# Optimization experiments

Hardware: AMD Instinct MI355X
Metric: run time of the kernel (lower is better)

## Reference

```python
import jax, jax.numpy as jnp
import numpy as np

N, K, E = 262144, 8, 16
DT = 0.02  # config.delta_time


def _mono(x, w1, b1, w2, b2):
    # monotonic_fun with increasing=False: out_linear(exp(-in_linear(x)))
    return jnp.exp(-(x @ w1.T + b1)) @ w2.T + b2


def _isin(a, b):
    # rowwise torch.isin: a [N,P], b [N,Q] -> [N,P] bool
    return (a[:, :, None] == b[:, None, :]).any(-1)


def _angle_clamp(vec, v, ang):
    # torch.cosine_similarity(v, vec, dim=-1).abs() > ang gate (eps=1e-8)
    num = jnp.einsum('nd,nrd->nr', v, vec)
    den = jnp.maximum(jnp.linalg.norm(v, axis=-1)[:, None] * jnp.linalg.norm(vec, axis=-1), 1e-8)
    keep = jnp.abs(num / den) > ang
    return jnp.where(keep[..., None], vec, 0.0)


def _linear_params(key, fan_in, fan_out):
    a = 1.0 / np.sqrt(fan_in)
    k1, k2 = jax.random.split(key)
    # weightConstraint(min_b=0) clamps weights to >= 0 at init
    w = jnp.maximum(jax.random.uniform(k1, (fan_out, fan_in), minval=-a, maxval=a), 0.0)
    b = jax.random.uniform(k2, (fan_out,), minval=-a, maxval=a)
    return w, b


def _mono_params(key):
    k1, k2 = jax.random.split(key)
    w1, b1 = _linear_params(k1, 1, E)
    w2, b2 = _linear_params(k2, E, 1)
    return w1, b1, w2, b2


def setup_inputs() -> dict:
    key = jax.random.key(0)
    ks = jax.random.split(key, 12)
    ego = jax.random.normal(ks[0], (N, 16), dtype=jnp.float32)
    ego = ego.at[:, 0].set(jnp.arange(N, dtype=jnp.float32))
    # surrounding-vehicle id columns 7..14 as small integer ids (floats)
    ego = ego.at[:, 7:15].set(jax.random.randint(ks[1], (N, 8), 0, 21).astype(jnp.float32))
    nei = jax.random.normal(ks[2], (N, K, 16), dtype=jnp.float32)
    nei = nei.at[:, :, 0].set(jax.random.randint(ks[3], (N, K), 1, 21).astype(jnp.float32))
    border = jax.random.uniform(ks[4], (4,), dtype=jnp.float32) * 10.0 + 1.0
    recording_time = jnp.zeros((N, K, 2), dtype=jnp.float32)
    p_dest = jax.random.uniform(ks[5], (2,), dtype=jnp.float32)  # relu(rand(2))
    angle = jax.nn.sigmoid(jax.random.uniform(ks[6], (1,), dtype=jnp.float32))
    d = {'ego': ego, 'nei': nei, 'border': border, 'recording_time': recording_time,
         'p_dest': p_dest, 'angle': angle}
    for name, kk in (('rep', ks[7]), ('att', ks[8]), ('bor', ks[9]), ('del', ks[10])):
        w1, b1, w2, b2 = _mono_params(kk)
        d[name + '_w1'], d[name + '_b1'], d[name + '_w2'], d[name + '_b2'] = w1, b1, w2, b2
    return d


def reference(ego, nei, border, recording_time, p_dest, angle,
              rep_w1, rep_b1, rep_w2, rep_b2,
              att_w1, att_b1, att_w2, att_b2,
              bor_w1, bor_b1, bor_w2, bor_b2,
              del_w1, del_b1, del_w2, del_b2):
    ang = angle[0]
    v = ego[:, 3:5]                                        # ego velocity [N,2]
    speed = jnp.linalg.norm(v, axis=-1)
    desired = jnp.stack([speed, jnp.zeros_like(speed)], axis=1)
    f_dest = ((p_dest[1] * desired - v) / p_dest[0])[:, None, :]   # [N,1,2]

    nei_id = nei[:, :, 0]                                  # [N,K]
    idx = _isin(nei_id, ego[:, 7:15]) & (nei_id != 0)

    # --- recording_time buffer update (vectorized remain/new/pad concat) ---
    buf_id, buf_ct = recording_time[:, :, 0], recording_time[:, :, 1]
    ifin = _isin(buf_id, nei_id)                           # buffer slots still present
    ct2 = buf_ct + ifin.astype(buf_ct.dtype)               # increment their counts
    ifnew = (~_isin(nei_id, buf_id)) & (nei_id != 0)       # brand-new neighbor ids
    cand = jnp.concatenate([jnp.stack([buf_id, ct2], -1),
                            jnp.stack([nei_id, jnp.ones_like(nei_id)], -1)], axis=1)  # [N,2K,2]
    ar = jnp.arange(K)
    BIG = 1 << 20
    keyord = jnp.concatenate([jnp.where(ifin, ar, BIG), jnp.where(ifnew, ar + K, BIG)], axis=1)
    order = jnp.argsort(keyord, axis=1)[:, :K]             # stable: remain order, then new, then pad
    skey = jnp.take_along_axis(keyord, order, axis=1)
    new_buf = jnp.where((skey < BIG)[..., None],
                        jnp.take_along_axis(cand, order[..., None], axis=1), 1.0)  # pad with ones
    count = new_buf[:, :, 1]                               # [N,K]

    # --- neighbor attraction / repulsion ---
    r = jnp.where(idx[..., None], nei[:, :, 1:3] - ego[:, None, 1:3], 0.0)
    rn = jnp.linalg.norm(r, axis=-1)
    rns = jnp.where(idx, rn, 1.0)                          # safe divisor (masked slots zeroed below)
    dirn = r / rns[..., None]
    f_attr = (_mono(count[..., None], del_w1, del_b1, del_w2, del_b2)
              * _mono(rn[..., None], att_w1, att_b1, att_w2, att_b2) * dirn)
    v_nei = nei[:, :, 3:5]
    b = rn + jnp.sum((r + v_nei * DT) ** 2, -1) - jnp.sum((v_nei * DT) ** 2, -1)
    b = jnp.sqrt(jnp.maximum(jnp.where(idx, b, 1.0), 1e-12)) / 2.0
    f_repu = _mono(b[..., None], rep_w1, rep_b1, rep_w2, rep_b2) * dirn
    f_attr = jnp.where(idx[..., None], f_attr, 0.0)
    f_repu = jnp.where(idx[..., None], f_repu, 0.0)

    # --- border repulsion (y-axis only), select_lane = [0, -1] ---
    rb_all = ego[:, 2:3] - border                          # [N,4]
    rb = jnp.stack([rb_all[:, 0], rb_all[:, -1]], axis=1)  # [N,2]
    rbn = jnp.abs(rb)
    f_by = _mono(rbn[..., None], bor_w1, bor_b1, bor_w2, bor_b2) * (rb / rbn)[..., None]
    f_bor = jnp.concatenate([jnp.zeros_like(f_by), f_by], axis=-1)  # [N,2,2]

    f_destination = _angle_clamp(f_dest, v, ang).sum(1)
    f_neighbors = _angle_clamp(f_attr, v, ang).sum(1) + _angle_clamp(f_repu, v, ang).sum(1)
    f_border = _angle_clamp(f_bor, v, ang).sum(1)
    return jnp.stack([f_destination, f_neighbors, f_border], axis=1)  # [N,3,2]
```

## Files before the change

### kernel.cpp

```cpp
#include <hip/hip_runtime.h>
#include <math.h>

#define KN 8
#define EN 16

__device__ __forceinline__ float mono_eval(float x,
    const float* __restrict__ w1, const float* __restrict__ b1,
    const float* __restrict__ w2, float b2) {
    float acc = 0.0f;
#pragma unroll
    for (int e = 0; e < EN; ++e) {
        float pre = x * w1[e] + b1[e];
        acc += expf(-pre) * w2[e];
    }
    return acc + b2;
}

__device__ __forceinline__ void clamp_add(float vx, float vy, float vnorm, float ang,
                                          float fx, float fy, float& ax, float& ay) {
    float num = vx * fx + vy * fy;
    float fn  = sqrtf(fx * fx + fy * fy);
    float den = fmaxf(vnorm * fn, 1e-8f);
    float c   = num / den;
    if (fabsf(c) > ang) { ax += fx; ay += fy; }
}

extern "C" __global__ void __launch_bounds__(256)
sfm_kernel(const float* __restrict__ ego, const float* __restrict__ nei,
           const float* __restrict__ border, const float* __restrict__ rec,
           const float* __restrict__ p_dest, const float* __restrict__ angle,
           const float* __restrict__ rep_w1, const float* __restrict__ rep_b1,
           const float* __restrict__ rep_w2, const float* __restrict__ rep_b2,
           const float* __restrict__ att_w1, const float* __restrict__ att_b1,
           const float* __restrict__ att_w2, const float* __restrict__ att_b2,
           const float* __restrict__ bor_w1, const float* __restrict__ bor_b1,
           const float* __restrict__ bor_w2, const float* __restrict__ bor_b2,
           const float* __restrict__ del_w1, const float* __restrict__ del_b1,
           const float* __restrict__ del_w2, const float* __restrict__ del_b2,
           float* __restrict__ out, int N)
{
    int n = blockIdx.x * blockDim.x + threadIdx.x;
    if (n >= N) return;

    const float ang = angle[0];
    const float p0 = p_dest[0], p1 = p_dest[1];
    const float b0 = border[0], b3 = border[3];

    const float4* e4 = (const float4*)(ego + (size_t)n * 16);
    float4 ea = e4[0], eb = e4[1], ec = e4[2], ed = e4[3];
    const float px_e = ea.y, py_e = ea.z;
    const float vx = ea.w, vy = eb.x;
    float egid[8] = {eb.w, ec.x, ec.y, ec.z, ec.w, ed.x, ed.y, ed.z};

    const float speed = sqrtf(vx * vx + vy * vy);

    float fdx = (p1 * speed - vx) / p0;
    float fdy = (0.0f - vy) / p0;
    float fdestx = 0.0f, fdesty = 0.0f;
    clamp_add(vx, vy, speed, ang, fdx, fdy, fdestx, fdesty);

    const float* nb = nei + (size_t)n * (KN * 16);
    float nid[KN], nx_[KN], ny_[KN], nvx[KN], nvy[KN];
#pragma unroll
    for (int k = 0; k < KN; ++k) {
        float4 a = *(const float4*)(nb + k * 16);
        nid[k] = a.x; nx_[k] = a.y; ny_[k] = a.z; nvx[k] = a.w;
        nvy[k] = nb[k * 16 + 4];
    }

    const float* rbuf = rec + (size_t)n * (KN * 2);
    float bid[KN], bct[KN];
#pragma unroll
    for (int k = 0; k < KN; k += 2) {
        float4 t = *(const float4*)(rbuf + k * 2);
        bid[k] = t.x; bct[k] = t.y; bid[k + 1] = t.z; bct[k + 1] = t.w;
    }

    float cnt[KN];
#pragma unroll
    for (int k = 0; k < KN; ++k) cnt[k] = 1.0f;
    int slot = 0;
#pragma unroll
    for (int k = 0; k < KN; ++k) {
        bool fin = false;
#pragma unroll
        for (int j = 0; j < KN; ++j) fin |= (bid[k] == nid[j]);
        if (fin) {
            float v2 = bct[k] + 1.0f;
#pragma unroll
            for (int s = 0; s < KN; ++s) if (slot == s) cnt[s] = v2;
            slot++;
        }
    }
#pragma unroll
    for (int k = 0; k < KN; ++k) {
        bool inbuf = false;
#pragma unroll
        for (int j = 0; j < KN; ++j) inbuf |= (nid[k] == bid[j]);
        bool isnew = (!inbuf) && (nid[k] != 0.0f);
        if (isnew) {
#pragma unroll
            for (int s = 0; s < KN; ++s) if (slot == s) cnt[s] = 1.0f;
            slot++;
        }
    }

    const float del_one = mono_eval(1.0f, del_w1, del_b1, del_w2, del_b2[0]);

    float fax_acc = 0.0f, fay_acc = 0.0f;
    float frx_acc = 0.0f, fry_acc = 0.0f;
#pragma unroll
    for (int k = 0; k < KN; ++k) {
        bool match = false;
#pragma unroll
        for (int j = 0; j < 8; ++j) match |= (nid[k] == egid[j]);
        const bool idxk = match && (nid[k] != 0.0f);

        float rx = idxk ? (nx_[k] - px_e) : 0.0f;
        float ry = idxk ? (ny_[k] - py_e) : 0.0f;
        float rn = sqrtf(rx * rx + ry * ry);
        float rns = idxk ? rn : 1.0f;
        float dx = rx / rns, dy = ry / rns;

        float att = mono_eval(rn, att_w1, att_b1, att_w2, att_b2[0]);
        float del = (cnt[k] == 1.0f) ? del_one
                  : mono_eval(cnt[k], del_w1, del_b1, del_w2, del_b2[0]);
        float fax = del * att * dx;
        float fay = del * att * dy;
        if (!idxk) { fax = 0.0f; fay = 0.0f; }
        clamp_add(vx, vy, speed, ang, fax, fay, fax_acc, fay_acc);

        float sx = nvx[k] * 0.02f, sy = nvy[k] * 0.02f;
        float ox = rx + sx, oy = ry + sy;
        float bsum = rn + (ox * ox + oy * oy) - (sx * sx + sy * sy);
        float bgate = idxk ? bsum : 1.0f;
        float bb = sqrtf(fmaxf(bgate, 1e-12f)) / 2.0f;

        float rep = mono_eval(bb, rep_w1, rep_b1, rep_w2, rep_b2[0]);
        float frx = rep * dx, fry = rep * dy;
        if (!idxk) { frx = 0.0f; fry = 0.0f; }
        clamp_add(vx, vy, speed, ang, frx, fry, frx_acc, fry_acc);
    }

    float fbx_acc = 0.0f, fby_acc = 0.0f;
    float rbv0 = py_e - b0, rbv1 = py_e - b3;
#pragma unroll
    for (int r = 0; r < 2; ++r) {
        float rb = (r == 0) ? rbv0 : rbv1;
        float rbn = fabsf(rb);
        float m = mono_eval(rbn, bor_w1, bor_b1, bor_w2, bor_b2[0]);
        float fby = m * (rb / rbn);
        clamp_add(vx, vy, speed, ang, 0.0f, fby, fbx_acc, fby_acc);
    }

    float2* o = (float2*)(out + (size_t)n * 6);
    o[0] = make_float2(fdestx, fdesty);
    o[1] = make_float2(fax_acc + frx_acc, fay_acc + fry_acc);
    o[2] = make_float2(fbx_acc, fby_acc);
}

extern "C" void kernel_launch(void* const* d_in, const int* in_sizes, int n_in,
                              void* d_out, int out_size, void* d_ws, size_t ws_size,
                              hipStream_t stream) {
    const float* ego    = (const float*)d_in[0];
    const float* nei    = (const float*)d_in[1];
    const float* border = (const float*)d_in[2];
    const float* rec    = (const float*)d_in[3];
    const float* p_dest = (const float*)d_in[4];
    const float* angle  = (const float*)d_in[5];
    const float* rep_w1 = (const float*)d_in[6];
    const float* rep_b1 = (const float*)d_in[7];
    const float* rep_w2 = (const float*)d_in[8];
    const float* rep_b2 = (const float*)d_in[9];
    const float* att_w1 = (const float*)d_in[10];
    const float* att_b1 = (const float*)d_in[11];
    const float* att_w2 = (const float*)d_in[12];
    const float* att_b2 = (const float*)d_in[13];
    const float* bor_w1 = (const float*)d_in[14];
    const float* bor_b1 = (const float*)d_in[15];
    const float* bor_w2 = (const float*)d_in[16];
    const float* bor_b2 = (const float*)d_in[17];
    const float* del_w1 = (const float*)d_in[18];
    const float* del_b1 = (const float*)d_in[19];
    const float* del_w2 = (const float*)d_in[20];
    const float* del_b2 = (const float*)d_in[21];
    float* out = (float*)d_out;

    int N = in_sizes[0] / 16;
    dim3 grid((N + 255) / 256);
    sfm_kernel<<<grid, 256, 0, stream>>>(
        ego, nei, border, rec, p_dest, angle,
        rep_w1, rep_b1, rep_w2, rep_b2,
        att_w1, att_b1, att_w2, att_b2,
        bor_w1, bor_b1, bor_w2, bor_b2,
        del_w1, del_b1, del_w2, del_b2,
        out, N);
}
```

Baseline: 268.0 us.

## Split each agent across 8 lanes, one neighbor per lane, with wave shuffles

Maps one thread per (agent, neighbor) pair instead of one thread per agent. The recording-buffer count compaction now uses ballot/popc/shuffle, and the per-agent sums are reduced with xor shuffles. The goal is 8x more parallelism and coalesced neighbor loads for a kernel bound by transcendentals and latency. The exp calls also switch to fast __expf with fma, which trades some accuracy. Each lane redundantly reloads the ego row, and the count-1 shortcut for the del network is dropped, so every lane evaluates it.

```diff
diff --git a/kernel.cpp b/kernel.cpp
--- a/kernel.cpp
+++ b/kernel.cpp
@@ -1,28 +1,18 @@
 #include <hip/hip_runtime.h>
 #include <math.h>
 
-#define KN 8
 #define EN 16
 
-__device__ __forceinline__ float mono_eval(float x,
+__device__ __forceinline__ float mono_fast(float x,
     const float* __restrict__ w1, const float* __restrict__ b1,
-    const float* __restrict__ w2, float b2) {
+    const float* __restrict__ w2, const float* __restrict__ b2) {
     float acc = 0.0f;
 #pragma unroll
     for (int e = 0; e < EN; ++e) {
-        float pre = x * w1[e] + b1[e];
-        acc += expf(-pre) * w2[e];
+        float pre = fmaf(x, w1[e], b1[e]);
+        acc = fmaf(__expf(-pre), w2[e], acc);
     }
-    return acc + b2;
-}
-
-__device__ __forceinline__ void clamp_add(float vx, float vy, float vnorm, float ang,
-                                          float fx, float fy, float& ax, float& ay) {
-    float num = vx * fx + vy * fy;
-    float fn  = sqrtf(fx * fx + fy * fy);
-    float den = fmaxf(vnorm * fn, 1e-8f);
-    float c   = num / den;
-    if (fabsf(c) > ang) { ax += fx; ay += fy; }
+    return acc + b2[0];
 }
 
 extern "C" __global__ void __launch_bounds__(256)
@@ -39,124 +29,125 @@
            const float* __restrict__ del_w2, const float* __restrict__ del_b2,
            float* __restrict__ out, int N)
 {
-    int n = blockIdx.x * blockDim.x + threadIdx.x;
+    const int gid = blockIdx.x * blockDim.x + threadIdx.x;
+    const int n = gid >> 3;
+    const int k = gid & 7;
     if (n >= N) return;
+    const int lane = threadIdx.x & 63;
+    const int gbase = lane & ~7;
 
     const float ang = angle[0];
     const float p0 = p_dest[0], p1 = p_dest[1];
-    const float b0 = border[0], b3 = border[3];
 
-    const float4* e4 = (const float4*)(ego + (size_t)n * 16);
-    float4 ea = e4[0], eb = e4[1], ec = e4[2], ed = e4[3];
-    const float px_e = ea.y, py_e = ea.z;
-    const float vx = ea.w, vy = eb.x;
-    float egid[8] = {eb.w, ec.x, ec.y, ec.z, ec.w, ed.x, ed.y, ed.z};
+    const float* er = ego + (size_t)n * 16;
+    float4 ea = *(const float4*)(er);
+    float4 eb = *(const float4*)(er + 4);
+    float4 ec = *(const float4*)(er + 8);
+    float4 ed = *(const float4*)(er + 12);
+    const float px = ea.y, py = ea.z, vx = ea.w, vy = eb.x;
+    const float speed = sqrtf(vx * vx + vy * vy);
 
-    const float speed = sqrtf(vx * vx + vy * vy);
+    const float* nb = nei + (size_t)n * 128 + (size_t)k * 16;
+    float4 na = *(const float4*)nb;
+    const float nvyv = nb[4];
+    const float nid = na.x;
+
+    float2 rc = *(const float2*)(rec + (size_t)n * 16 + (size_t)k * 2);
+    const float bid = rc.x, bct = rc.y;
+
+    bool fin = (bid == nid);
+#pragma unroll
+    for (int t = 1; t < 8; ++t)
+        fin = fin || (bid == __shfl_xor(nid, t));
+
+    unsigned long long bal = __ballot(fin);
+    unsigned finM = (unsigned)((bal >> gbase) & 0xFFull);
+    int popcFin = __popc(finM);
+    int jsel = 0, cbits = 0;
+#pragma unroll
+    for (int j = 0; j < 8; ++j) {
+        int bit = (finM >> j) & 1;
+        if (bit && cbits == k) jsel = j;
+        cbits += bit;
+    }
+    float bctj = __shfl(bct, gbase + jsel);
+    float cntk = (k < popcFin) ? (bctj + 1.0f) : 1.0f;
+
+    bool match = (nid == eb.w) || (nid == ec.x) || (nid == ec.y) || (nid == ec.z)
+              || (nid == ec.w) || (nid == ed.x) || (nid == ed.y) || (nid == ed.z);
+    const bool idxk = match && (nid != 0.0f);
+
+    float rx = idxk ? (na.y - px) : 0.0f;
+    float ry = idxk ? (na.z - py) : 0.0f;
+    float rn = sqrtf(rx * rx + ry * ry);
+    float rns = idxk ? rn : 1.0f;
+    float dx = rx / rns, dy = ry / rns;
+
+    float att = mono_fast(rn,   att_w1, att_b1, att_w2, att_b2);
+    float del = mono_fast(cntk, del_w1, del_b1, del_w2, del_b2);
+    float sa = del * att;
+    float fax = idxk ? sa * dx : 0.0f;
+    float fay = idxk ? sa * dy : 0.0f;
+
+    float nbx = 0.0f, nby = 0.0f;
+    {
+        float num = vx * fax + vy * fay;
+        float fn = sqrtf(fax * fax + fay * fay);
+        float den = fmaxf(speed * fn, 1e-8f);
+        if (fabsf(num / den) > ang) { nbx += fax; nby += fay; }
+    }
+
+    float sxv = na.w * 0.02f, syv = nvyv * 0.02f;
+    float ox = rx + sxv, oy = ry + syv;
+    float bsum = rn + (ox * ox + oy * oy) - (sxv * sxv + syv * syv);
+    float bgate = idxk ? bsum : 1.0f;
+    float bb = sqrtf(fmaxf(bgate, 1e-12f)) * 0.5f;
+    float rep = mono_fast(bb, rep_w1, rep_b1, rep_w2, rep_b2);
+    float frx = idxk ? rep * dx : 0.0f;
+    float fry = idxk ? rep * dy : 0.0f;
+    {
+        float num = vx * frx + vy * fry;
+        float fn = sqrtf(frx * frx + fry * fry);
+        float den = fmaxf(speed * fn, 1e-8f);
+        if (fabsf(num / den) > ang) { nbx += frx; nby += fry; }
+    }
+
+    float bsel = (k == 0) ? border[0] : border[3];
+    float rb = py - bsel;
+    float rbn = fabsf(rb);
+    float mb = mono_fast(rbn, bor_w1, bor_b1, bor_w2, bor_b2);
+    float fby = mb * (rb / rbn);
+    float bory = 0.0f;
+    {
+        float num = vy * fby;
+        float den = fmaxf(speed * fabsf(fby), 1e-8f);
+        if ((fabsf(num / den) > ang) && (k < 2)) bory = fby;
+    }
+
+#pragma unroll
+    for (int m = 1; m < 8; m <<= 1) {
+        nbx  += __shfl_xor(nbx,  m);
+        nby  += __shfl_xor(nby,  m);
+        bory += __shfl_xor(bory, m);
+    }
 
     float fdx = (p1 * speed - vx) / p0;
     float fdy = (0.0f - vy) / p0;
-    float fdestx = 0.0f, fdesty = 0.0f;
-    clamp_add(vx, vy, speed, ang, fdx, fdy, fdestx, fdesty);
-
-    const float* nb = nei + (size_t)n * (KN * 16);
-    float nid[KN], nx_[KN], ny_[KN], nvx[KN], nvy[KN];
-#pragma unroll
-    for (int k = 0; k < KN; ++k) {
-        float4 a = *(const float4*)(nb + k * 16);
-        nid[k] = a.x; nx_[k] = a.y; ny_[k] = a.z; nvx[k] = a.w;
-        nvy[k] = nb[k * 16 + 4];
+    float fdex = 0.0f, fdey = 0.0f;
+    {
+        float num = vx * fdx + vy * fdy;
+        float fn = sqrtf(fdx * fdx + fdy * fdy);
+        float den = fmaxf(speed * fn, 1e-8f);
+        if (fabsf(num / den) > ang) { fdex = fdx; fdey = fdy; }
     }
 
-    const float* rbuf = rec + (size_t)n * (KN * 2);
-    float bid[KN], bct[KN];
-#pragma unroll
-    for (int k = 0; k < KN; k += 2) {
-        float4 t = *(const float4*)(rbuf + k * 2);
-        bid[k] = t.x; bct[k] = t.y; bid[k + 1] = t.z; bct[k + 1] = t.w;
-    }
-
-    float cnt[KN];
-#pragma unroll
-    for (int k = 0; k < KN; ++k) cnt[k] = 1.0f;
-    int slot = 0;
-#pragma unroll
-    for (int k = 0; k < KN; ++k) {
-        bool fin = false;
-#pragma unroll
-        for (int j = 0; j < KN; ++j) fin |= (bid[k] == nid[j]);
-        if (fin) {
-            float v2 = bct[k] + 1.0f;
-#pragma unroll
-            for (int s = 0; s < KN; ++s) if (slot == s) cnt[s] = v2;
-            slot++;
-        }
-    }
-#pragma unroll
-    for (int k = 0; k < KN; ++k) {
-        bool inbuf = false;
-#pragma unroll
-        for (int j = 0; j < KN; ++j) inbuf |= (nid[k] == bid[j]);
-        bool isnew = (!inbuf) && (nid[k] != 0.0f);
-        if (isnew) {
-#pragma unroll
-            for (int s = 0; s < KN; ++s) if (slot == s) cnt[s] = 1.0f;
-            slot++;
-        }
-    }
-
-    const float del_one = mono_eval(1.0f, del_w1, del_b1, del_w2, del_b2[0]);
-
-    float fax_acc = 0.0f, fay_acc = 0.0f;
-    float frx_acc = 0.0f, fry_acc = 0.0f;
-#pragma unroll
-    for (int k = 0; k < KN; ++k) {
-        bool match = false;
-#pragma unroll
-        for (int j = 0; j < 8; ++j) match |= (nid[k] == egid[j]);
-        const bool idxk = match && (nid[k] != 0.0f);
-
-        float rx = idxk ? (nx_[k] - px_e) : 0.0f;
-        float ry = idxk ? (ny_[k] - py_e) : 0.0f;
-        float rn = sqrtf(rx * rx + ry * ry);
-        float rns = idxk ? rn : 1.0f;
-        float dx = rx / rns, dy = ry / rns;
-
-        float att = mono_eval(rn, att_w1, att_b1, att_w2, att_b2[0]);
-        float del = (cnt[k] == 1.0f) ? del_one
-                  : mono_eval(cnt[k], del_w1, del_b1, del_w2, del_b2[0]);
-        float fax = del * att * dx;
-        float fay = del * att * dy;
-        if (!idxk) { fax = 0.0f; fay = 0.0f; }
-        clamp_add(vx, vy, speed, ang, fax, fay, fax_acc, fay_acc);
-
-        float sx = nvx[k] * 0.02f, sy = nvy[k] * 0.02f;
-        float ox = rx + sx, oy = ry + sy;
-        float bsum = rn + (ox * ox + oy * oy) - (sx * sx + sy * sy);
-        float bgate = idxk ? bsum : 1.0f;
-        float bb = sqrtf(fmaxf(bgate, 1e-12f)) / 2.0f;
-
-        float rep = mono_eval(bb, rep_w1, rep_b1, rep_w2, rep_b2[0]);
-        float frx = rep * dx, fry = rep * dy;
-        if (!idxk) { frx = 0.0f; fry = 0.0f; }
-        clamp_add(vx, vy, speed, ang, frx, fry, frx_acc, fry_acc);
-    }
-
-    float fbx_acc = 0.0f, fby_acc = 0.0f;
-    float rbv0 = py_e - b0, rbv1 = py_e - b3;
-#pragma unroll
-    for (int r = 0; r < 2; ++r) {
-        float rb = (r == 0) ? rbv0 : rbv1;
-        float rbn = fabsf(rb);
-        float m = mono_eval(rbn, bor_w1, bor_b1, bor_w2, bor_b2[0]);
-        float fby = m * (rb / rbn);
-        clamp_add(vx, vy, speed, ang, 0.0f, fby, fbx_acc, fby_acc);
-    }
-
-    float2* o = (float2*)(out + (size_t)n * 6);
-    o[0] = make_float2(fdestx, fdesty);
-    o[1] = make_float2(fax_acc + frx_acc, fay_acc + fry_acc);
-    o[2] = make_float2(fbx_acc, fby_acc);
+    float wv = (k == 0) ? fdex
+             : (k == 1) ? fdey
+             : (k == 2) ? nbx
+             : (k == 3) ? nby
+             : (k == 4) ? 0.0f
+             : bory;
+    if (k < 6) out[(size_t)n * 6 + k] = wv;
 }
 
 extern "C" void kernel_launch(void* const* d_in, const int* in_sizes, int n_in,
@@ -187,7 +178,8 @@
     float* out = (float*)d_out;
 
     int N = in_sizes[0] / 16;
-    dim3 grid((N + 255) / 256);
+    long long threads = (long long)N * 8;
+    dim3 grid((unsigned)((threads + 255) / 256));
     sfm_kernel<<<grid, 256, 0, stream>>>(
         ego, nei, border, rec, p_dest, angle,
         rep_w1, rep_b1, rep_w2, rep_b2,
```

After: 251.5 us. 1.07x faster.
